# Kernel optimization log

Hardware: AMD Instinct MI355X
Metric: run time of the kernel (lower is better)

The kernel has to match this reference:

```python
import jax, jax.numpy as jnp
import numpy as np

HIDDEN = 1280
HEADS = 16
HEAD_DIM = HIDDEN // HEADS  # 80
TOTAL = 8192
N_CHUNKS = 8


def rotate_half(x):
    x1, x2 = jnp.split(x, 2, axis=-1)
    return jnp.concatenate([-x2, x1], axis=-1)


def setup_inputs() -> dict:
    key = jax.random.key(0)
    ks = jax.random.split(key, 7)
    hidden_states = jax.random.normal(ks[0], (TOTAL, HIDDEN), dtype=jnp.float32)
    cos = jax.random.uniform(ks[1], (TOTAL, HEAD_DIM), dtype=jnp.float32)
    sin = jax.random.uniform(ks[2], (TOTAL, HEAD_DIM), dtype=jnp.float32)
    s = 1.0 / np.sqrt(HIDDEN)
    w_qkv = jax.random.normal(ks[3], (HIDDEN, 3 * HIDDEN), dtype=jnp.float32) * s
    b_qkv = jax.random.normal(ks[4], (3 * HIDDEN,), dtype=jnp.float32) * 0.01
    w_proj = jax.random.normal(ks[5], (HIDDEN, HIDDEN), dtype=jnp.float32) * s
    b_proj = jax.random.normal(ks[6], (HIDDEN,), dtype=jnp.float32) * 0.01
    return {"hidden_states": hidden_states, "cos": cos, "sin": sin,
            "w_qkv": w_qkv, "b_qkv": b_qkv, "w_proj": w_proj,
            "b_proj": b_proj, "n_chunks": N_CHUNKS}


def reference(hidden_states, cos, sin, w_qkv, b_qkv, w_proj, b_proj, n_chunks):
    T, D = hidden_states.shape
    C = int(n_chunks)
    L = T // C  # equal-length chunks (block-diagonal varlen attention)
    H, hd = HEADS, HEAD_DIM
    scale = hd ** -0.5

    qkv = hidden_states @ w_qkv + b_qkv                    # [T, 3D]
    q, k, v = jnp.split(qkv, 3, axis=-1)
    # [C, L, H, hd]
    q = q.reshape(C, L, H, hd)
    k = k.reshape(C, L, H, hd)
    v = v.reshape(C, L, H, hd)
    cos_c = cos.reshape(C, L, 1, hd)
    sin_c = sin.reshape(C, L, 1, hd)
    q = q * cos_c + rotate_half(q) * sin_c
    k = k * cos_c + rotate_half(k) * sin_c

    # block-diagonal attention: each chunk attends only within itself
    scores = jnp.einsum('clhd,cmhd->chlm', q, k) * scale   # [C, H, L, L]
    weights = jax.nn.softmax(scores.astype(jnp.float32), axis=-1).astype(v.dtype)
    attn = jnp.einsum('chlm,cmhd->clhd', weights, v)       # [C, L, H, hd]
    attn = attn.reshape(T, D)
    return attn @ w_proj + b_proj
```

## Files before the change

kernel.cpp:

```cpp
#include <hip/hip_runtime.h>

#define T_TOK 8192
#define D_HID 1280
#define H_    16
#define HD_   80
#define C_    8
#define L_    1024
#define N3_   3840
#define QPAD  96

typedef _Float16 f16;
typedef __attribute__((ext_vector_type(8))) _Float16 h8;
typedef __attribute__((ext_vector_type(4))) float f32x4;

__global__ __launch_bounds__(256) void convert_x(const float* __restrict__ x,
                                                 f16* __restrict__ y) {
  const int g = blockIdx.x * 256 + threadIdx.x;
  const float4 v = ((const float4*)x)[g];
  f16 o[4] = {(f16)v.x, (f16)v.y, (f16)v.z, (f16)v.w};
  ((uint2*)y)[g] = *(const uint2*)o;
}

__global__ __launch_bounds__(256) void convert_w_t(const float* __restrict__ W,
                                                   f16* __restrict__ Wt,
                                                   int K, int N) {
  __shared__ float tile[32][33];
  const int n0 = blockIdx.x * 32, k0 = blockIdx.y * 32;
  const int c = threadIdx.x & 31, r0 = threadIdx.x >> 5;
#pragma unroll
  for (int it = 0; it < 4; ++it) {
    const int r = r0 + it * 8;
    tile[r][c] = W[(size_t)(k0 + r) * N + n0 + c];
  }
  __syncthreads();
#pragma unroll
  for (int it = 0; it < 4; ++it) {
    const int r = r0 + it * 8;
    Wt[(size_t)(n0 + r) * K + k0 + c] = (f16)tile[c][r];
  }
}

__device__ __forceinline__ void stage_half(const f16* __restrict__ gpanel, int K,
                                           f16* sdst, int t, int half) {
#pragma unroll
  for (int r = 0; r < 2; ++r) {
    const int s = r * 512 + (int)threadIdx.x;
    const int row = half * 128 + (s >> 3);
    const int part = (s & 7) ^ (row & 7);
    const f16* gp = gpanel + (size_t)row * K + t * 64 + part * 8;
    __builtin_amdgcn_global_load_lds(
        (const __attribute__((address_space(1))) void*)gp,
        (__attribute__((address_space(3))) void*)(sdst + row * 64 + (s & 7) * 8),
        16, 0, 0);
  }
}

__device__ __forceinline__ h8 fragld64(const f16* s, int row, int c) {
  const int slot = c ^ (row & 7);
  return *(const h8*)&s[row * 64 + slot * 8];
}

__global__ __launch_bounds__(512, 2) void gemm_f16(
    const f16* __restrict__ A, const f16* __restrict__ B,
    const float* __restrict__ bias,
    float* __restrict__ Cf, f16* __restrict__ Ch,
    int M, int N, int K) {
  __shared__ f16 sAB[2][2][256 * 64];
  const int tid = threadIdx.x;
  const int wave = tid >> 6, lane = tid & 63;
  const int quad = lane >> 4, ln = lane & 15;

  const int nwg = gridDim.x;
  int wg = blockIdx.x;
  wg = (wg & 7) * (nwg >> 3) + (wg >> 3);
  const int nbx = N >> 8;
  const int bm = (wg / nbx) * 256, bn = (wg % nbx) * 256;
  const int wm = (wave >> 2) * 128, wn = (wave & 3) * 64;

  f32x4 acc[8][4];
#pragma unroll
  for (int i = 0; i < 8; ++i)
#pragma unroll
    for (int j = 0; j < 4; ++j) acc[i][j] = (f32x4){0.f, 0.f, 0.f, 0.f};

  const f16* Abase = A + (size_t)bm * K;
  const f16* Bbase = B + (size_t)bn * K;
  const int nt = K >> 6;

  stage_half(Abase, K, sAB[0][0], 0, 0);
  stage_half(Abase, K, sAB[0][0], 0, 1);
  stage_half(Bbase, K, sAB[0][1], 0, 0);
  stage_half(Bbase, K, sAB[0][1], 0, 1);
  stage_half(Abase, K, sAB[1][0], 1, 0);
  stage_half(Abase, K, sAB[1][0], 1, 1);
  asm volatile("s_waitcnt vmcnt(4)" ::: "memory");
  __builtin_amdgcn_sched_barrier(0);
  __builtin_amdgcn_s_barrier();

  for (int t = 0; t < nt; ++t) {
    const f16* sA = sAB[t & 1][0];
    const f16* sB = sAB[t & 1][1];
    const int nb = (t + 1) & 1;
    h8 af[4][2], af2[4][2], bf01[2][2], bf23[2][2];

#pragma unroll
    for (int i = 0; i < 4; ++i)
#pragma unroll
      for (int ks = 0; ks < 2; ++ks)
        af[i][ks] = fragld64(sA, wm + i * 16 + ln, ks * 4 + quad);
#pragma unroll
    for (int j = 0; j < 2; ++j)
#pragma unroll
      for (int ks = 0; ks < 2; ++ks)
        bf01[j][ks] = fragld64(sB, wn + j * 16 + ln, ks * 4 + quad);
#pragma unroll
    for (int j = 0; j < 2; ++j)
#pragma unroll
      for (int ks = 0; ks < 2; ++ks)
        bf23[j][ks] = fragld64(sB, wn + (j + 2) * 16 + ln, ks * 4 + quad);
    if (t + 1 < nt) stage_half(Bbase, K, sAB[nb][1], t + 1, 0);

    __builtin_amdgcn_s_setprio(1);
#pragma unroll
    for (int ks = 0; ks < 2; ++ks)
#pragma unroll
      for (int i = 0; i < 4; ++i)
#pragma unroll
        for (int j = 0; j < 2; ++j)
          acc[i][j] = __builtin_amdgcn_mfma_f32_16x16x32_f16(af[i][ks], bf01[j][ks], acc[i][j], 0, 0, 0);
    __builtin_amdgcn_s_setprio(0);

#pragma unroll
    for (int i = 0; i < 4; ++i)
#pragma unroll
      for (int ks = 0; ks < 2; ++ks)
        af2[i][ks] = fragld64(sA, wm + (i + 4) * 16 + ln, ks * 4 + quad);
    if (t + 1 < nt) stage_half(Bbase, K, sAB[nb][1], t + 1, 1);

    __builtin_amdgcn_s_setprio(1);
#pragma unroll
    for (int ks = 0; ks < 2; ++ks)
#pragma unroll
      for (int i = 0; i < 4; ++i)
#pragma unroll
        for (int j = 0; j < 2; ++j)
          acc[i][j + 2] = __builtin_amdgcn_mfma_f32_16x16x32_f16(af[i][ks], bf23[j][ks], acc[i][j + 2], 0, 0, 0);
    __builtin_amdgcn_s_setprio(0);

    asm volatile("s_waitcnt lgkmcnt(0)" ::: "memory");
    __builtin_amdgcn_sched_barrier(0);
    __builtin_amdgcn_s_barrier();
    if (t + 2 < nt) {
      stage_half(Abase, K, sAB[t & 1][0], t + 2, 0);
      stage_half(Abase, K, sAB[t & 1][0], t + 2, 1);
    }

    __builtin_amdgcn_s_setprio(1);
#pragma unroll
    for (int ks = 0; ks < 2; ++ks)
#pragma unroll
      for (int i = 0; i < 4; ++i)
#pragma unroll
        for (int j = 0; j < 2; ++j)
          acc[i + 4][j + 2] = __builtin_amdgcn_mfma_f32_16x16x32_f16(af2[i][ks], bf23[j][ks], acc[i + 4][j + 2], 0, 0, 0);
#pragma unroll
    for (int ks = 0; ks < 2; ++ks)
#pragma unroll
      for (int i = 0; i < 4; ++i)
#pragma unroll
        for (int j = 0; j < 2; ++j)
          acc[i + 4][j] = __builtin_amdgcn_mfma_f32_16x16x32_f16(af2[i][ks], bf01[j][ks], acc[i + 4][j], 0, 0, 0);
    __builtin_amdgcn_s_setprio(0);

    if (t + 1 < nt) {
      if (t + 2 < nt) asm volatile("s_waitcnt vmcnt(4)" ::: "memory");
      else            asm volatile("s_waitcnt vmcnt(0)" ::: "memory");
      __builtin_amdgcn_sched_barrier(0);
      __builtin_amdgcn_s_barrier();
    }
  }

  float bv[4];
#pragma unroll
  for (int j = 0; j < 4; ++j) bv[j] = bias[bn + wn + j * 16 + ln];
#pragma unroll
  for (int i = 0; i < 8; ++i)
#pragma unroll
    for (int j = 0; j < 4; ++j)
#pragma unroll
      for (int r = 0; r < 4; ++r) {
        const int row = bm + wm + i * 16 + quad * 4 + r;
        const int col = bn + wn + j * 16 + ln;
        const float val = acc[i][j][r] + bv[j];
        if (Ch) Ch[(size_t)row * N + col] = (f16)val;
        else    Cf[(size_t)row * N + col] = val;
      }
}

__global__ __launch_bounds__(256) void rope_convert(
    const f16* __restrict__ qkv, const float* __restrict__ cosb,
    const float* __restrict__ sinb, f16* __restrict__ Qb, f16* __restrict__ Kb) {
  const int tid = threadIdx.x;
  const int wave = tid >> 6, lane = tid & 63;
  const int t = blockIdx.x * 4 + wave;
  const size_t rowb = (size_t)t * N3_;
  const float qscale = 0.11180339887498949f;
#pragma unroll
  for (int u = 0; u < 5; ++u) {
    const int g = u * 64 + lane;
    const int e = g * 8;
    const int d = e % HD_;
    const int h = (e % D_HID) / HD_;
    const bool isK = e >= D_HID;
    const bool lo = d < 40;
    const int pe = lo ? e + 40 : e - 40;
    f16 v[8], p[8];
    *(int4*)v = *(const int4*)(qkv + rowb + e);
    *(int4*)p = *(const int4*)(qkv + rowb + pe);
    const float4 cs0 = *(const float4*)(cosb + (size_t)t * HD_ + d);
    const float4 cs1 = *(const float4*)(cosb + (size_t)t * HD_ + d + 4);
    const float4 sn0 = *(const float4*)(sinb + (size_t)t * HD_ + d);
    const float4 sn1 = *(const float4*)(sinb + (size_t)t * HD_ + d + 4);
    const float cs[8] = {cs0.x, cs0.y, cs0.z, cs0.w, cs1.x, cs1.y, cs1.z, cs1.w};
    const float sn[8] = {sn0.x, sn0.y, sn0.z, sn0.w, sn1.x, sn1.y, sn1.z, sn1.w};
    f16 o[8];
#pragma unroll
    for (int j = 0; j < 8; ++j) {
      const float pv = lo ? -(float)p[j] : (float)p[j];
      const float ov = (float)v[j] * cs[j] + pv * sn[j];
      o[j] = (f16)(isK ? ov : ov * qscale);
    }
    *(int4*)((isK ? Kb : Qb) + ((size_t)h * T_TOK + t) * QPAD + d) = *(const int4*)o;
  }
  {
    const int qk = lane >> 5, h = (lane >> 1) & 15, half = lane & 1;
    f16* dst = (qk ? Kb : Qb) + ((size_t)h * T_TOK + t) * QPAD + 80 + half * 8;
    *(int4*)dst = make_int4(0, 0, 0, 0);
  }
}

__global__ __launch_bounds__(256) void vt_convert(const f16* __restrict__ qkv,
                                                  f16* __restrict__ Vt) {
  __shared__ f16 tl[HD_][136];
  const int h = blockIdx.x & 15;
  const int t0 = (blockIdx.x >> 4) * 128;
  const int tid = threadIdx.x;
#pragma unroll
  for (int it = 0; it < 5; ++it) {
    const int e = tid + it * 256;
    const int t = e / 10, pc = e % 10;
    int4 v = *(const int4*)(qkv + (size_t)(t0 + t) * N3_ + 2 * D_HID + h * HD_ + pc * 8);
    f16 tmp[8];
    *(int4*)tmp = v;
#pragma unroll
    for (int u = 0; u < 8; ++u) tl[pc * 8 + u][t] = tmp[u];
  }
  __syncthreads();
#pragma unroll
  for (int it = 0; it < 5; ++it) {
    const int e = tid + it * 256;
    const int d = e >> 4, pt = e & 15;
    *(int4*)(Vt + ((size_t)h * HD_ + d) * T_TOK + t0 + pt * 8) = *(const int4*)&tl[d][pt * 8];
  }
}

__global__ __launch_bounds__(256, 2) void attn_flash(
    const f16* __restrict__ Qb, const f16* __restrict__ Kb,
    const f16* __restrict__ Vt, f16* __restrict__ Oa) {
  __shared__ f16 Ps[4][64][72];
  const int tid = threadIdx.x;
  const int wave = tid >> 6, lane = tid & 63;
  const int quad = lane >> 4, ln = lane & 15;
  const int h = blockIdx.x & 15;
  const int qb = (blockIdx.x >> 4) & 3;
  const int c = blockIdx.x >> 6;
  const int t0 = c * L_ + qb * 256 + wave * 64;
  const size_t hb = (size_t)h * T_TOK;

  h8 aq[4][3];
#pragma unroll
  for (int i = 0; i < 4; ++i)
#pragma unroll
    for (int ks = 0; ks < 3; ++ks)
      aq[i][ks] = *(const h8*)(Qb + (hb + t0 + i * 16 + ln) * QPAD + ks * 32 + quad * 8);

  f32x4 o[4][5];
  float lsum[4][4];
#pragma unroll
  for (int i = 0; i < 4; ++i) {
#pragma unroll
    for (int jn = 0; jn < 5; ++jn) o[i][jn] = (f32x4){0.f, 0.f, 0.f, 0.f};
#pragma unroll
    for (int r = 0; r < 4; ++r) lsum[i][r] = 0.f;
  }

  for (int kb = 0; kb < 16; ++kb) {
    const int kt0 = c * L_ + kb * 64;
#pragma unroll
    for (int j = 0; j < 4; ++j) {
      h8 bk[3];
#pragma unroll
      for (int ks = 0; ks < 3; ++ks)
        bk[ks] = *(const h8*)(Kb + (hb + kt0 + j * 16 + ln) * QPAD + ks * 32 + quad * 8);
      f32x4 s[4];
#pragma unroll
      for (int i = 0; i < 4; ++i) s[i] = (f32x4){0.f, 0.f, 0.f, 0.f};
      __builtin_amdgcn_s_setprio(1);
#pragma unroll
      for (int ks = 0; ks < 3; ++ks)
#pragma unroll
        for (int i = 0; i < 4; ++i)
          s[i] = __builtin_amdgcn_mfma_f32_16x16x32_f16(aq[i][ks], bk[ks], s[i], 0, 0, 0);
      __builtin_amdgcn_s_setprio(0);
#pragma unroll
      for (int i = 0; i < 4; ++i)
#pragma unroll
        for (int r = 0; r < 4; ++r) {
          const float p = __expf(s[i][r]);
          lsum[i][r] += p;
          Ps[wave][i * 16 + quad * 4 + r][j * 16 + ln] = (f16)p;
        }
    }
#pragma unroll
    for (int ks = 0; ks < 2; ++ks) {
      h8 ap[4];
#pragma unroll
      for (int i = 0; i < 4; ++i)
        ap[i] = *(const h8*)&Ps[wave][i * 16 + ln][ks * 32 + quad * 8];
#pragma unroll
      for (int jn = 0; jn < 5; ++jn) {
        const h8 bv = *(const h8*)(Vt + ((size_t)h * HD_ + jn * 16 + ln) * T_TOK
                                   + kt0 + ks * 32 + quad * 8);
        __builtin_amdgcn_s_setprio(1);
#pragma unroll
        for (int i = 0; i < 4; ++i)
          o[i][jn] = __builtin_amdgcn_mfma_f32_16x16x32_f16(ap[i], bv, o[i][jn], 0, 0, 0);
        __builtin_amdgcn_s_setprio(0);
      }
    }
  }

#pragma unroll
  for (int i = 0; i < 4; ++i)
#pragma unroll
    for (int r = 0; r < 4; ++r) {
      float s = lsum[i][r];
#pragma unroll
      for (int off = 1; off < 16; off <<= 1) s += __shfl_xor(s, off);
      lsum[i][r] = 1.f / s;
    }

#pragma unroll
  for (int i = 0; i < 4; ++i)
#pragma unroll
    for (int r = 0; r < 4; ++r) {
      const int t = t0 + i * 16 + quad * 4 + r;
      const float inv = lsum[i][r];
#pragma unroll
      for (int jn = 0; jn < 5; ++jn)
        Oa[(size_t)t * D_HID + h * HD_ + jn * 16 + ln] = (f16)(o[i][jn][r] * inv);
    }
}

extern "C" void kernel_launch(void* const* d_in, const int* in_sizes, int n_in,
                              void* d_out, int out_size, void* d_ws, size_t ws_size,
                              hipStream_t stream) {
  (void)in_sizes; (void)n_in; (void)out_size; (void)ws_size;
  const float* x      = (const float*)d_in[0];
  const float* cosb   = (const float*)d_in[1];
  const float* sinb   = (const float*)d_in[2];
  const float* w_qkv  = (const float*)d_in[3];
  const float* b_qkv  = (const float*)d_in[4];
  const float* w_proj = (const float*)d_in[5];
  const float* b_proj = (const float*)d_in[6];
  float* out = (float*)d_out;

  char* ws = (char*)d_ws;
  f16* qkv_h  = (f16*)(ws);
  f16* attn_h = (f16*)(ws);
  f16* x_h    = (f16*)(ws + 62914560);
  f16* Qb     = (f16*)(ws + 62914560);
  f16* Kb     = (f16*)(ws + 88080384);
  f16* Vt     = (f16*)(ws + 113246208);
  f16* wq_t   = (f16*)(ws + 134217728);
  f16* wp_t   = (f16*)(ws + 144048128);

  convert_x<<<(T_TOK * D_HID / 4) / 256, 256, 0, stream>>>(x, x_h);
  convert_w_t<<<dim3(N3_ / 32, D_HID / 32), 256, 0, stream>>>(w_qkv, wq_t, D_HID, N3_);
  convert_w_t<<<dim3(D_HID / 32, D_HID / 32), 256, 0, stream>>>(w_proj, wp_t, D_HID, D_HID);
  gemm_f16<<<(N3_ / 256) * (T_TOK / 256), 512, 0, stream>>>(
      x_h, wq_t, b_qkv, nullptr, qkv_h, T_TOK, N3_, D_HID);
  rope_convert<<<T_TOK / 4, 256, 0, stream>>>(qkv_h, cosb, sinb, Qb, Kb);
  vt_convert<<<H_ * (T_TOK / 128), 256, 0, stream>>>(qkv_h, Vt);
  attn_flash<<<C_ * 4 * H_, 256, 0, stream>>>(Qb, Kb, Vt, attn_h);
  gemm_f16<<<(D_HID / 256) * (T_TOK / 256), 512, 0, stream>>>(
      attn_h, wp_t, b_proj, out, nullptr, T_TOK, D_HID, D_HID);
}
```

Measured before the change: 362.6 us.

## Keep softmax probabilities in registers by transposing QK^T MFMA operands

Swaps the A/B operands of the QK^T MFMA so each lane's score accumulator lines up with the A-operand layout of a 16x16x16 MFMA. The exp'd probabilities then feed P·V straight from registers instead of being written to and read back from a shared-memory tile. The row-sum reduction is rewritten for the transposed layout, and the V loads shrink to 4-wide. In exchange, P·V uses twice as many smaller MFMA instructions, and each wave holds more registers for the probability fragments.

```diff
diff --git a/kernel.cpp b/kernel.cpp
--- a/kernel.cpp
+++ b/kernel.cpp
@@ -11,6 +11,7 @@
 
 typedef _Float16 f16;
 typedef __attribute__((ext_vector_type(8))) _Float16 h8;
+typedef __attribute__((ext_vector_type(4))) _Float16 h4;
 typedef __attribute__((ext_vector_type(4))) float f32x4;
 
 __global__ __launch_bounds__(256) void convert_x(const float* __restrict__ x,
@@ -267,7 +268,6 @@
 __global__ __launch_bounds__(256, 2) void attn_flash(
     const f16* __restrict__ Qb, const f16* __restrict__ Kb,
     const f16* __restrict__ Vt, f16* __restrict__ Oa) {
-  __shared__ f16 Ps[4][64][72];
   const int tid = threadIdx.x;
   const int wave = tid >> 6, lane = tid & 63;
   const int quad = lane >> 4, ln = lane & 15;
@@ -285,17 +285,17 @@
       aq[i][ks] = *(const h8*)(Qb + (hb + t0 + i * 16 + ln) * QPAD + ks * 32 + quad * 8);
 
   f32x4 o[4][5];
-  float lsum[4][4];
+  float lsum[4];
 #pragma unroll
   for (int i = 0; i < 4; ++i) {
 #pragma unroll
     for (int jn = 0; jn < 5; ++jn) o[i][jn] = (f32x4){0.f, 0.f, 0.f, 0.f};
-#pragma unroll
-    for (int r = 0; r < 4; ++r) lsum[i][r] = 0.f;
+    lsum[i] = 0.f;
   }
 
   for (int kb = 0; kb < 16; ++kb) {
     const int kt0 = c * L_ + kb * 64;
+    h4 pa[4][4];
 #pragma unroll
     for (int j = 0; j < 4; ++j) {
       h8 bk[3];
@@ -310,52 +310,47 @@
       for (int ks = 0; ks < 3; ++ks)
 #pragma unroll
         for (int i = 0; i < 4; ++i)
-          s[i] = __builtin_amdgcn_mfma_f32_16x16x32_f16(aq[i][ks], bk[ks], s[i], 0, 0, 0);
+          s[i] = __builtin_amdgcn_mfma_f32_16x16x32_f16(bk[ks], aq[i][ks], s[i], 0, 0, 0);
       __builtin_amdgcn_s_setprio(0);
 #pragma unroll
-      for (int i = 0; i < 4; ++i)
-#pragma unroll
-        for (int r = 0; r < 4; ++r) {
-          const float p = __expf(s[i][r]);
-          lsum[i][r] += p;
-          Ps[wave][i * 16 + quad * 4 + r][j * 16 + ln] = (f16)p;
-        }
-    }
-#pragma unroll
-    for (int ks = 0; ks < 2; ++ks) {
-      h8 ap[4];
-#pragma unroll
-      for (int i = 0; i < 4; ++i)
-        ap[i] = *(const h8*)&Ps[wave][i * 16 + ln][ks * 32 + quad * 8];
+      for (int i = 0; i < 4; ++i) {
+        const float e0 = __expf(s[i][0]);
+        const float e1 = __expf(s[i][1]);
+        const float e2 = __expf(s[i][2]);
+        const float e3 = __expf(s[i][3]);
+        lsum[i] += (e0 + e1) + (e2 + e3);
+        pa[i][j] = (h4){(f16)e0, (f16)e1, (f16)e2, (f16)e3};
+      }
+    }
+#pragma unroll
+    for (int kk = 0; kk < 4; ++kk) {
 #pragma unroll
       for (int jn = 0; jn < 5; ++jn) {
-        const h8 bv = *(const h8*)(Vt + ((size_t)h * HD_ + jn * 16 + ln) * T_TOK
-                                   + kt0 + ks * 32 + quad * 8);
+        const h4 bv = *(const h4*)(Vt + ((size_t)h * HD_ + jn * 16 + ln) * T_TOK
+                                   + kt0 + kk * 16 + quad * 4);
         __builtin_amdgcn_s_setprio(1);
 #pragma unroll
         for (int i = 0; i < 4; ++i)
-          o[i][jn] = __builtin_amdgcn_mfma_f32_16x16x32_f16(ap[i], bv, o[i][jn], 0, 0, 0);
+          o[i][jn] = __builtin_amdgcn_mfma_f32_16x16x16f16(pa[i][kk], bv, o[i][jn], 0, 0, 0);
         __builtin_amdgcn_s_setprio(0);
       }
     }
   }
 
 #pragma unroll
-  for (int i = 0; i < 4; ++i)
-#pragma unroll
-    for (int r = 0; r < 4; ++r) {
-      float s = lsum[i][r];
-#pragma unroll
-      for (int off = 1; off < 16; off <<= 1) s += __shfl_xor(s, off);
-      lsum[i][r] = 1.f / s;
-    }
+  for (int i = 0; i < 4; ++i) {
+    float s = lsum[i];
+    s += __shfl_xor(s, 16);
+    s += __shfl_xor(s, 32);
+    lsum[i] = s;
+  }
 
 #pragma unroll
   for (int i = 0; i < 4; ++i)
 #pragma unroll
     for (int r = 0; r < 4; ++r) {
       const int t = t0 + i * 16 + quad * 4 + r;
-      const float inv = lsum[i][r];
+      const float inv = 1.f / __shfl(lsum[i], quad * 4 + r);
 #pragma unroll
       for (int jn = 0; jn < 5; ++jn)
         Oa[(size_t)t * D_HID + h * HD_ + jn * 16 + ln] = (f16)(o[i][jn][r] * inv);
```

Result: slower. 397.5 us (+9.6%).
